# Kernel optimization log

Hardware: AMD Instinct MI355X
Metric: run time of the kernel (lower is better)

## Reference

```python
import jax, jax.numpy as jnp
import numpy as np

B, C, H, W = 32, 256, 64, 64
M, D = 256, 512           # memory_size, memory_dim
NH, HD = 8, 64            # heads, head_dim
EPS = 1e-5


def setup_inputs() -> dict:
    key = jax.random.key(0)
    ks = jax.random.split(key, 12)
    s = 0.02
    return {
        "x": jax.random.normal(ks[0], (B, C, H, W), jnp.float32),
        "memory_bank": jax.random.normal(ks[1], (M, D), jnp.float32),
        "enc_conv_w": jax.random.normal(ks[2], (D // 2, C), jnp.float32) * s,  # 1x1 conv == channel matmul
        "enc_conv_b": jnp.zeros((D // 2,), jnp.float32),
        "bn_gamma": jnp.ones((D // 2,), jnp.float32),
        "bn_beta": jnp.zeros((D // 2,), jnp.float32),
        "bn_mean": jnp.zeros((D // 2,), jnp.float32),
        "bn_var": jnp.ones((D // 2,), jnp.float32),
        "enc_lin_w": jax.random.normal(ks[3], (D, D // 2), jnp.float32) * s,
        "enc_lin_b": jnp.zeros((D,), jnp.float32),
        "ln_gamma": jnp.ones((D,), jnp.float32),
        "ln_beta": jnp.zeros((D,), jnp.float32),
        "attn_in_w": jax.random.normal(ks[4], (3 * D, D), jnp.float32) * s,
        "attn_in_b": jnp.zeros((3 * D,), jnp.float32),
        "attn_out_w": jax.random.normal(ks[5], (D, D), jnp.float32) * s,
        "attn_out_b": jnp.zeros((D,), jnp.float32),
        "gate_w": jax.random.normal(ks[6], (D, 2 * D), jnp.float32) * s,
        "gate_b": jnp.zeros((D,), jnp.float32),
        "rec_w1": jax.random.normal(ks[7], (D // 2, D), jnp.float32) * s,
        "rec_b1": jnp.zeros((D // 2,), jnp.float32),
        "rec_w2": jax.random.normal(ks[8], (C, D // 2), jnp.float32) * s,
        "rec_b2": jnp.zeros((C,), jnp.float32),
        "spat_conv_w": jax.random.normal(ks[9], (1, 2, 7, 7), jnp.float32) * s,
    }


def reference(x, memory_bank, enc_conv_w, enc_conv_b, bn_gamma, bn_beta, bn_mean, bn_var,
              enc_lin_w, enc_lin_b, ln_gamma, ln_beta, attn_in_w, attn_in_b,
              attn_out_w, attn_out_b, gate_w, gate_b, rec_w1, rec_b1, rec_w2, rec_b2,
              spat_conv_w):
    # ---- feature encoder: 1x1 conv -> BN(eval) -> ReLU -> global avg pool -> Linear -> LayerNorm ----
    h = jnp.einsum('bchw,oc->bohw', x, enc_conv_w) + enc_conv_b[None, :, None, None]
    bn_scale = (bn_gamma / jnp.sqrt(bn_var + EPS))[None, :, None, None]
    h = (h - bn_mean[None, :, None, None]) * bn_scale + bn_beta[None, :, None, None]
    h = jax.nn.relu(h)
    h = h.mean(axis=(2, 3))                                   # (B, D//2)
    h = h @ enc_lin_w.T + enc_lin_b                           # (B, D)
    mu = h.mean(-1, keepdims=True)
    var = h.var(-1, keepdims=True)
    enc = (h - mu) / jnp.sqrt(var + EPS) * ln_gamma + ln_beta  # (B, D)

    # ---- memory retrieval: MHA with q_len=1, keys/values = shared memory bank ----
    Wq, Wk, Wv = jnp.split(attn_in_w, 3, axis=0)
    bq, bk, bv = jnp.split(attn_in_b, 3)
    q = (enc @ Wq.T + bq).reshape(B, NH, HD)                  # (B, H, d)
    k = (memory_bank @ Wk.T + bk).reshape(M, NH, HD)          # (M, H, d) — batch-shared
    v = (memory_bank @ Wv.T + bv).reshape(M, NH, HD)
    scores = jnp.einsum('bhd,mhd->bhm', q, k) / np.float32(np.sqrt(HD))
    att = jax.nn.softmax(scores, axis=-1)                     # (B, H, M)
    ctx = jnp.einsum('bhm,mhd->bhd', att, v).reshape(B, D)
    retrieved = ctx @ attn_out_w.T + attn_out_b               # (B, D)

    # ---- gated fusion ----
    gate = jax.nn.sigmoid(jnp.concatenate([enc, retrieved], axis=-1) @ gate_w.T + gate_b)
    fused = gate * enc + (1.0 - gate) * retrieved             # (B, D)

    # ---- per-channel weights from fused features ----
    sw = jax.nn.sigmoid(jax.nn.relu(fused @ rec_w1.T + rec_b1) @ rec_w2.T + rec_b2)  # (B, C)

    # ---- spatial attention on [avg, max] channel stats ----
    avg = x.mean(axis=1, keepdims=True)
    mx = x.max(axis=1, keepdims=True)
    sp_in = jnp.concatenate([avg, mx], axis=1)                # (B, 2, H, W)
    sa = jax.lax.conv_general_dilated(sp_in, spat_conv_w, (1, 1), [(3, 3), (3, 3)],
                                      dimension_numbers=('NCHW', 'OIHW', 'NCHW'))
    sa = jax.nn.sigmoid(sa)                                   # (B, 1, H, W)

    return x * sw[:, :, None, None] * sa                      # (B, C, H, W)
```

## Files before the change

kernel.cpp:

```cpp
#include <hip/hip_runtime.h>
#include <math.h>

#define EPSV 1e-5f

typedef __attribute__((ext_vector_type(8))) short short8;
typedef __attribute__((ext_vector_type(8))) unsigned short ushort8;
typedef __attribute__((ext_vector_type(4))) float f32x4;

__device__ __forceinline__ unsigned short f2bf(float f){
  unsigned u = __builtin_bit_cast(unsigned, f);
  u += 0x7fffu + ((u >> 16) & 1u);
  return (unsigned short)(u >> 16);
}
__device__ __forceinline__ float dot4f(float4 w, const float* v){
  return w.x*v[0] + w.y*v[1] + w.z*v[2] + w.w*v[3];
}
__device__ __forceinline__ float sigmoidf(float v){ return 1.f/(1.f + expf(-v)); }

__global__ __launch_bounds__(256) void k_pack(const float* __restrict__ w1,
                                              const float* __restrict__ wattn,
                                              unsigned short* __restrict__ p1,
                                              unsigned short* __restrict__ pkv){
  const int total1 = 256*256, total2 = 1024*512;
  for (int idx = blockIdx.x*256 + threadIdx.x; idx < total1 + total2; idx += gridDim.x*256){
    if (idx < total1){
      int o = idx >> 8, c = idx & 255;
      int off = (((o>>4)*8 + (c>>5))*64 + (((c>>3)&3)*16 + (o&15)))*8 + (c&7);
      p1[off] = f2bf(w1[idx]);
    } else {
      int j = idx - total1; int o = j >> 9, c = j & 511;
      int off = (((o>>4)*16 + (c>>5))*64 + (((c>>3)&3)*16 + (o&15)))*8 + (c&7);
      pkv[off] = f2bf(wattn[512*512 + j]);
    }
  }
}

__global__ __launch_bounds__(256) void k_conv(
    const float* __restrict__ x, const unsigned short* __restrict__ wp,
    const float* __restrict__ cb, const float* __restrict__ bng,
    const float* __restrict__ bnb, const float* __restrict__ bnm,
    const float* __restrict__ bnv,
    float* __restrict__ ppool, float* __restrict__ wavg, float* __restrict__ wmax){
  int bid = blockIdx.x;
  int b = bid >> 6, tile = bid & 63;
  int px0 = tile << 6;
  int t = threadIdx.x;
  int lane = t & 63, wv = t >> 6;
  int px = t & 63, cg = wv;
  __shared__ __align__(16) unsigned short a_lds[16384];
  __shared__ float st_s[256], st_m[256];

  const float* xb = x + (size_t)b*(256*4096) + px0 + px;

  float ssum = 0.f, smax = -3.4e38f;
  const unsigned wbase = (((px >> 4) << 6) + ((unsigned)cg << 4) + (px & 15)) << 4;

  #pragma unroll
  for (int ch = 0; ch < 8; ++ch){
    float xv[8];
    #pragma unroll
    for (int u = 0; u < 8; ++u)
      xv[u] = __builtin_nontemporal_load(xb + (size_t)(ch*32 + cg*8 + u) * 4096);
    ushort8 pk;
    #pragma unroll
    for (int u = 0; u < 8; ++u){
      ssum += xv[u];
      smax = fmaxf(smax, xv[u]);
      pk[u] = f2bf(xv[u]);
    }
    *(ushort8*)((char*)a_lds + wbase + (ch << 12)) = pk;
  }
  st_s[t] = ssum; st_m[t] = smax;
  __syncthreads();

  if (t < 64){
    float s = st_s[t] + st_s[t+64] + st_s[t+128] + st_s[t+192];
    float m = fmaxf(fmaxf(st_m[t], st_m[t+64]), fmaxf(st_m[t+128], st_m[t+192]));
    wavg[(b << 12) + px0 + t] = s * (1.f/256.f);
    wmax[(b << 12) + px0 + t] = m;
  }

  f32x4 acc[4][4];
  #pragma unroll
  for (int i = 0; i < 4; ++i)
    #pragma unroll
    for (int j = 0; j < 4; ++j){ f32x4 z = {0.f,0.f,0.f,0.f}; acc[i][j] = z; }

  #pragma unroll
  for (int ch = 0; ch < 8; ++ch){
    short8 afr[4];
    #pragma unroll
    for (int mf = 0; mf < 4; ++mf)
      afr[mf] = *(const short8*)((const char*)a_lds + (ch << 12) + (mf << 10) + lane*16);
    #pragma unroll
    for (int nf = 0; nf < 4; ++nf){
      short8 bfr = *(const short8*)(wp + (size_t)(((wv*4 + nf)*8 + ch) * 512 + lane*8));
      #pragma unroll
      for (int mf = 0; mf < 4; ++mf)
        acc[mf][nf] = __builtin_amdgcn_mfma_f32_16x16x32_bf16(afr[mf], bfr, acc[mf][nf], 0, 0, 0);
    }
  }

  #pragma unroll
  for (int nf = 0; nf < 4; ++nf){
    int o = (wv << 6) + (nf << 4) + (lane & 15);
    float sc = bng[o] * rsqrtf(bnv[o] + EPSV);
    float sh = bnb[o] + (cb[o] - bnm[o]) * sc;
    float ps = 0.f;
    #pragma unroll
    for (int mf = 0; mf < 4; ++mf)
      #pragma unroll
      for (int r = 0; r < 4; ++r)
        ps += fmaxf(acc[mf][nf][r] * sc + sh, 0.f);
    ps += __shfl_xor(ps, 16, 64);
    ps += __shfl_xor(ps, 32, 64);
    if ((lane & 48) == 0)
      ppool[(size_t)((b << 6) + tile)*256 + o] = ps;
  }
}

__global__ __launch_bounds__(256) void k_enc(const float* __restrict__ pp,
    const float* __restrict__ lw, const float* __restrict__ lb,
    const float* __restrict__ lng, const float* __restrict__ lnb,
    float* __restrict__ enc){
  int b = blockIdx.x, t = threadIdx.x;
  __shared__ __align__(16) float p_s[256];
  __shared__ float h_s[512], red[8];
  float s = 0.f;
  for (int tile = 0; tile < 64; ++tile) s += pp[(size_t)((b<<6)+tile)*256 + t];
  p_s[t] = s * (1.f/4096.f);
  __syncthreads();
  float hv[2];
  #pragma unroll
  for (int k = 0; k < 2; ++k){
    int d = t + k*256;
    const float4* wr = (const float4*)(lw + (size_t)d*256);
    float a = 0.f;
    for (int j = 0; j < 64; ++j) a += dot4f(wr[j], &p_s[4*j]);
    hv[k] = a + lb[d];
    h_s[d] = hv[k];
  }
  float ls = hv[0] + hv[1], lq = hv[0]*hv[0] + hv[1]*hv[1];
  #pragma unroll
  for (int msk = 1; msk < 64; msk <<= 1){
    ls += __shfl_xor(ls, msk, 64);
    lq += __shfl_xor(lq, msk, 64);
  }
  if ((t & 63) == 0){ red[t>>6] = ls; red[4 + (t>>6)] = lq; }
  __syncthreads();
  float su = red[0]+red[1]+red[2]+red[3];
  float sq = red[4]+red[5]+red[6]+red[7];
  float mu = su * (1.f/512.f);
  float vr = sq * (1.f/512.f) - mu*mu;
  float rstd = rsqrtf(vr + EPSV);
  #pragma unroll
  for (int k = 0; k < 2; ++k){
    int d = t + k*256;
    enc[(size_t)b*512 + d] = (h_s[d] - mu)*rstd*lng[d] + lnb[d];
  }
}

__global__ __launch_bounds__(256) void k_kv(const float* __restrict__ mb,
    const unsigned short* __restrict__ wp, const float* __restrict__ attb,
    float* __restrict__ kvb){
  int bid = blockIdx.x;
  int mt = bid >> 4, nt = bid & 15;
  int m0 = mt << 4;
  int mu = nt >> 3;
  int ncol0 = (nt & 7) << 6;
  int t = threadIdx.x, lane = t & 63, wv = t >> 6;
  int l15 = lane & 15, l4 = lane >> 4;

  const float* arow = mb + (size_t)(m0 + l15)*512 + l4*8;
  int ofrag = (nt << 2) + wv;

  f32x4 acc = {0.f,0.f,0.f,0.f};
  #pragma unroll
  for (int ch = 0; ch < 16; ++ch){
    float4 a0 = *(const float4*)(arow + ch*32);
    float4 a1 = *(const float4*)(arow + ch*32 + 4);
    short8 afr;
    afr[0] = (short)f2bf(a0.x); afr[1] = (short)f2bf(a0.y);
    afr[2] = (short)f2bf(a0.z); afr[3] = (short)f2bf(a0.w);
    afr[4] = (short)f2bf(a1.x); afr[5] = (short)f2bf(a1.y);
    afr[6] = (short)f2bf(a1.z); afr[7] = (short)f2bf(a1.w);
    short8 bfr = *(const short8*)(wp + (size_t)(ofrag*16 + ch)*512 + lane*8);
    acc = __builtin_amdgcn_mfma_f32_16x16x32_bf16(afr, bfr, acc, 0, 0, 0);
  }
  float bias = attb[512 + mu*512 + ncol0 + (wv << 4) + l15];
  #pragma unroll
  for (int i = 0; i < 4; ++i){
    int row = m0 + l4*4 + i;
    int col = ncol0 + (wv << 4) + l15;
    kvb[(size_t)mu*131072 + (size_t)row*512 + col] = acc[i] + bias;
  }
}

__global__ __launch_bounds__(256) void k_qkattn(const float* __restrict__ enc,
    const float* __restrict__ kvb, const float* __restrict__ attw,
    const float* __restrict__ attb, float* __restrict__ ctxout){
  int bid = blockIdx.x;
  int b = bid >> 3, h = bid & 7;
  int t = threadIdx.x;
  __shared__ float e_s[512];
  __shared__ __align__(16) float q_s[64];
  __shared__ float att_s[256];
  __shared__ float red_s[256];
  __shared__ float r2[8];

  e_s[t]       = enc[(size_t)b*512 + t];
  e_s[t + 256] = enc[(size_t)b*512 + 256 + t];
  __syncthreads();

  {
    int i = t >> 2, part = t & 3;
    const float4* wr = (const float4*)(attw + (size_t)(h*64 + i)*512 + part*128);
    const float* ev = e_s + part*128;
    float a = 0.f;
    #pragma unroll
    for (int j = 0; j < 32; ++j) a += dot4f(wr[j], ev + 4*j);
    a += __shfl_xor(a, 1, 64);
    a += __shfl_xor(a, 2, 64);
    if (part == 0) q_s[i] = a + attb[h*64 + i];
  }
  __syncthreads();

  float sc;
  {
    const float4* kr = (const float4*)(kvb + (size_t)t*512 + h*64);
    const float4* qr = (const float4*)q_s;
    float a = 0.f;
    #pragma unroll
    for (int j = 0; j < 16; ++j){
      float4 kk = kr[j], qq = qr[j];
      a += kk.x*qq.x + kk.y*qq.y + kk.z*qq.z + kk.w*qq.w;
    }
    sc = a * 0.125f;
  }
  int wv = t >> 6, lane = t & 63;
  float mx = sc;
  #pragma unroll
  for (int msk = 1; msk < 64; msk <<= 1) mx = fmaxf(mx, __shfl_xor(mx, msk, 64));
  if (lane == 0) r2[wv] = mx;
  __syncthreads();
  mx = fmaxf(fmaxf(r2[0], r2[1]), fmaxf(r2[2], r2[3]));
  float ex = expf(sc - mx);
  float sum = ex;
  #pragma unroll
  for (int msk = 1; msk < 64; msk <<= 1) sum += __shfl_xor(sum, msk, 64);
  if (lane == 0) r2[4 + wv] = sum;
  __syncthreads();
  float inv = 1.f / (r2[4] + r2[5] + r2[6] + r2[7]);
  att_s[t] = ex * inv;
  __syncthreads();

  {
    const float* vbase = kvb + 131072 + (size_t)(wv*64)*512 + h*64 + lane;
    const float* at = att_s + wv*64;
    float a = 0.f;
    #pragma unroll 8
    for (int m = 0; m < 64; ++m) a += at[m] * vbase[(size_t)m*512];
    red_s[wv*64 + lane] = a;
  }
  __syncthreads();
  if (t < 64)
    ctxout[(size_t)b*512 + h*64 + t] = red_s[t] + red_s[64+t] + red_s[128+t] + red_s[192+t];
}

__global__ __launch_bounds__(256) void k_outproj(const float* __restrict__ ctx,
    const float* __restrict__ ow, const float* __restrict__ obv,
    float* __restrict__ retr){
  int bid = blockIdx.x;
  int b = bid >> 3, n0 = (bid & 7) << 6;
  int t = threadIdx.x;
  __shared__ float c_s[512];
  c_s[t]       = ctx[(size_t)b*512 + t];
  c_s[t + 256] = ctx[(size_t)b*512 + 256 + t];
  __syncthreads();
  int o = n0 + (t >> 2), part = t & 3;
  const float4* wr = (const float4*)(ow + (size_t)o*512 + part*128);
  const float* cv = c_s + part*128;
  float a = 0.f;
  #pragma unroll
  for (int j = 0; j < 32; ++j) a += dot4f(wr[j], cv + 4*j);
  a += __shfl_xor(a, 1, 64);
  a += __shfl_xor(a, 2, 64);
  if (part == 0) retr[(size_t)b*512 + o] = a + obv[o];
}

__global__ __launch_bounds__(256) void k_gate(const float* __restrict__ enc,
    const float* __restrict__ retr, const float* __restrict__ gw,
    const float* __restrict__ gb, float* __restrict__ fused){
  int bid = blockIdx.x;
  int b = bid >> 3, n0 = (bid & 7) << 6;
  int t = threadIdx.x;
  __shared__ float ef[1024];
  ef[t]        = enc[(size_t)b*512 + t];
  ef[t + 256]  = enc[(size_t)b*512 + 256 + t];
  ef[t + 512]  = retr[(size_t)b*512 + t];
  ef[t + 768]  = retr[(size_t)b*512 + 256 + t];
  __syncthreads();
  int o = n0 + (t >> 2), part = t & 3;
  const float4* wr = (const float4*)(gw + (size_t)o*1024 + part*256);
  const float* fv = ef + part*256;
  float a = 0.f;
  #pragma unroll
  for (int j = 0; j < 64; ++j) a += dot4f(wr[j], fv + 4*j);
  a += __shfl_xor(a, 1, 64);
  a += __shfl_xor(a, 2, 64);
  if (part == 0){
    float g = sigmoidf(a + gb[o]);
    fused[(size_t)b*512 + o] = g*ef[o] + (1.f - g)*ef[512 + o];
  }
}

__global__ __launch_bounds__(256) void k_rec1(const float* __restrict__ fused,
    const float* __restrict__ r1w, const float* __restrict__ r1b,
    float* __restrict__ t1){
  int bid = blockIdx.x;
  int b = bid >> 2, n0 = (bid & 3) << 6;
  int t = threadIdx.x;
  __shared__ float f_s[512];
  f_s[t]       = fused[(size_t)b*512 + t];
  f_s[t + 256] = fused[(size_t)b*512 + 256 + t];
  __syncthreads();
  int o = n0 + (t >> 2), part = t & 3;
  const float4* wr = (const float4*)(r1w + (size_t)o*512 + part*128);
  const float* fv = f_s + part*128;
  float a = 0.f;
  #pragma unroll
  for (int j = 0; j < 32; ++j) a += dot4f(wr[j], fv + 4*j);
  a += __shfl_xor(a, 1, 64);
  a += __shfl_xor(a, 2, 64);
  if (part == 0) t1[(size_t)b*256 + o] = fmaxf(a + r1b[o], 0.f);
}

__global__ __launch_bounds__(256) void k_rec2(const float* __restrict__ t1,
    const float* __restrict__ r2w, const float* __restrict__ r2b,
    float* __restrict__ swout){
  int bid = blockIdx.x;
  int b = bid >> 2, n0 = (bid & 3) << 6;
  int t = threadIdx.x;
  __shared__ float t_s[256];
  t_s[t] = t1[(size_t)b*256 + t];
  __syncthreads();
  int o = n0 + (t >> 2), part = t & 3;
  const float4* wr = (const float4*)(r2w + (size_t)o*256 + part*64);
  const float* tv = t_s + part*64;
  float a = 0.f;
  #pragma unroll
  for (int j = 0; j < 16; ++j) a += dot4f(wr[j], tv + 4*j);
  a += __shfl_xor(a, 1, 64);
  a += __shfl_xor(a, 2, 64);
  if (part == 0) swout[(size_t)b*256 + o] = sigmoidf(a + r2b[o]);
}

__global__ __launch_bounds__(256) void k_spconv(const float* __restrict__ wavg,
    const float* __restrict__ wmax, const float* __restrict__ wgt,
    float* __restrict__ sa){
  __shared__ float w_s[98];
  int t = threadIdx.x;
  if (t < 98) w_s[t] = wgt[t];
  __syncthreads();
  int b = blockIdx.x >> 4;
  int px = ((blockIdx.x & 15) << 8) + t;
  int y = px >> 6, xx = px & 63;
  const float* pa = wavg + (b << 12);
  const float* pm = wmax + (b << 12);
  float a = 0.f;
  #pragma unroll
  for (int ky = 0; ky < 7; ++ky){
    int yy = y + ky - 3;
    if (yy < 0 || yy >= 64) continue;
    #pragma unroll
    for (int kx = 0; kx < 7; ++kx){
      int x2 = xx + kx - 3;
      if (x2 < 0 || x2 >= 64) continue;
      int o = (yy << 6) + x2;
      a += pa[o]*w_s[ky*7+kx] + pm[o]*w_s[49+ky*7+kx];
    }
  }
  sa[(b << 12) + px] = sigmoidf(a);
}

__global__ __launch_bounds__(256) void k_final(const float* __restrict__ x,
    const float* __restrict__ sw, const float* __restrict__ sa,
    float* __restrict__ out){
  const size_t total = 8388608;
  for (size_t q = (size_t)blockIdx.x*256 + threadIdx.x; q < total; q += (size_t)gridDim.x*256){
    size_t b = q >> 18;
    int c = (int)((q >> 10) & 255);
    int p4 = (int)(q & 1023);
    f32x4 xv = __builtin_nontemporal_load((const f32x4*)x + q);
    f32x4 sv = ((const f32x4*)sa)[(b << 10) + p4];
    float s = sw[(b << 8) + c];
    f32x4 o = xv * s * sv;
    __builtin_nontemporal_store(o, (f32x4*)out + q);
  }
}

extern "C" void kernel_launch(void* const* d_in, const int* in_sizes, int n_in,
                              void* d_out, int out_size, void* d_ws, size_t ws_size,
                              hipStream_t stream){
  const float* x    = (const float*)d_in[0];
  const float* mb   = (const float*)d_in[1];
  const float* w1   = (const float*)d_in[2];
  const float* cbv  = (const float*)d_in[3];
  const float* bng  = (const float*)d_in[4];
  const float* bnb  = (const float*)d_in[5];
  const float* bnm  = (const float*)d_in[6];
  const float* bnv  = (const float*)d_in[7];
  const float* lw   = (const float*)d_in[8];
  const float* lb   = (const float*)d_in[9];
  const float* lng  = (const float*)d_in[10];
  const float* lnb  = (const float*)d_in[11];
  const float* attw = (const float*)d_in[12];
  const float* attb = (const float*)d_in[13];
  const float* ow   = (const float*)d_in[14];
  const float* obv  = (const float*)d_in[15];
  const float* gw   = (const float*)d_in[16];
  const float* gb   = (const float*)d_in[17];
  const float* r1w  = (const float*)d_in[18];
  const float* r1b  = (const float*)d_in[19];
  const float* r2w  = (const float*)d_in[20];
  const float* r2b  = (const float*)d_in[21];
  const float* spw  = (const float*)d_in[22];
  float* out = (float*)d_out;

  char* ws = (char*)d_ws;
  unsigned short* w1p  = (unsigned short*)(ws + 0);
  unsigned short* wkvp = (unsigned short*)(ws + 131072);
  float* ppool = (float*)(ws + 1179648);
  float* wavg  = (float*)(ws + 3276800);
  float* wmax  = (float*)(ws + 3801088);
  float* encb  = (float*)(ws + 4325376);
  float* kvb   = (float*)(ws + 4390912);
  float* swb   = (float*)(ws + 5439488);
  float* sab   = (float*)(ws + 5472256);
  float* ctxb  = (float*)(ws + 5996544);
  float* retrb = (float*)(ws + 6062080);
  float* fusedb= (float*)(ws + 6127616);
  float* t1b   = (float*)(ws + 6193152);

  k_pack   <<<2304, 256, 0, stream>>>(w1, attw, w1p, wkvp);
  k_conv   <<<2048, 256, 0, stream>>>(x, w1p, cbv, bng, bnb, bnm, bnv, ppool, wavg, wmax);
  k_enc    <<<32,   256, 0, stream>>>(ppool, lw, lb, lng, lnb, encb);
  k_kv     <<<256,  256, 0, stream>>>(mb, wkvp, attb, kvb);
  k_qkattn <<<256,  256, 0, stream>>>(encb, kvb, attw, attb, ctxb);
  k_outproj<<<256,  256, 0, stream>>>(ctxb, ow, obv, retrb);
  k_gate   <<<256,  256, 0, stream>>>(encb, retrb, gw, gb, fusedb);
  k_rec1   <<<128,  256, 0, stream>>>(fusedb, r1w, r1b, t1b);
  k_rec2   <<<128,  256, 0, stream>>>(t1b, r2w, r2b, swb);
  k_spconv <<<512,  256, 0, stream>>>(wavg, wmax, spw, sab);
  k_final  <<<2048, 256, 0, stream>>>(x, swb, sab, out);
}
```

Baseline: 176.6 us.

## Fuse encoder LayerNorm into attention and merge tail MLPs into one kernel

Removes the standalone encoder kernel by recomputing the pooled-feature linear plus LayerNorm inside each attention block. It also fuses out-projection, gating, and both reconstruction layers into a single per-batch 512-thread kernel. Four launches and the global round-trips of intermediates go away. In exchange the encoder matvec is computed redundantly eight times per batch, and the tail runs on only 32 blocks, each thread streaming full weight rows, so parallelism across the device is much lower.

```diff
diff --git a/kernel.cpp b/kernel.cpp
--- a/kernel.cpp
+++ b/kernel.cpp
@@ -119,47 +119,6 @@
   }
 }
 
-__global__ __launch_bounds__(256) void k_enc(const float* __restrict__ pp,
-    const float* __restrict__ lw, const float* __restrict__ lb,
-    const float* __restrict__ lng, const float* __restrict__ lnb,
-    float* __restrict__ enc){
-  int b = blockIdx.x, t = threadIdx.x;
-  __shared__ __align__(16) float p_s[256];
-  __shared__ float h_s[512], red[8];
-  float s = 0.f;
-  for (int tile = 0; tile < 64; ++tile) s += pp[(size_t)((b<<6)+tile)*256 + t];
-  p_s[t] = s * (1.f/4096.f);
-  __syncthreads();
-  float hv[2];
-  #pragma unroll
-  for (int k = 0; k < 2; ++k){
-    int d = t + k*256;
-    const float4* wr = (const float4*)(lw + (size_t)d*256);
-    float a = 0.f;
-    for (int j = 0; j < 64; ++j) a += dot4f(wr[j], &p_s[4*j]);
-    hv[k] = a + lb[d];
-    h_s[d] = hv[k];
-  }
-  float ls = hv[0] + hv[1], lq = hv[0]*hv[0] + hv[1]*hv[1];
-  #pragma unroll
-  for (int msk = 1; msk < 64; msk <<= 1){
-    ls += __shfl_xor(ls, msk, 64);
-    lq += __shfl_xor(lq, msk, 64);
-  }
-  if ((t & 63) == 0){ red[t>>6] = ls; red[4 + (t>>6)] = lq; }
-  __syncthreads();
-  float su = red[0]+red[1]+red[2]+red[3];
-  float sq = red[4]+red[5]+red[6]+red[7];
-  float mu = su * (1.f/512.f);
-  float vr = sq * (1.f/512.f) - mu*mu;
-  float rstd = rsqrtf(vr + EPSV);
-  #pragma unroll
-  for (int k = 0; k < 2; ++k){
-    int d = t + k*256;
-    enc[(size_t)b*512 + d] = (h_s[d] - mu)*rstd*lng[d] + lnb[d];
-  }
-}
-
 __global__ __launch_bounds__(256) void k_kv(const float* __restrict__ mb,
     const unsigned short* __restrict__ wp, const float* __restrict__ attb,
     float* __restrict__ kvb){
@@ -196,20 +155,56 @@
   }
 }
 
-__global__ __launch_bounds__(256) void k_qkattn(const float* __restrict__ enc,
+__global__ __launch_bounds__(256) void k_qkattn(const float* __restrict__ pp,
+    const float* __restrict__ lw, const float* __restrict__ lb,
+    const float* __restrict__ lng, const float* __restrict__ lnb,
     const float* __restrict__ kvb, const float* __restrict__ attw,
     const float* __restrict__ attb, float* __restrict__ ctxout){
   int bid = blockIdx.x;
   int b = bid >> 3, h = bid & 7;
   int t = threadIdx.x;
+  __shared__ __align__(16) float p_s[256];
   __shared__ float e_s[512];
   __shared__ __align__(16) float q_s[64];
   __shared__ float att_s[256];
   __shared__ float red_s[256];
   __shared__ float r2[8];
 
-  e_s[t]       = enc[(size_t)b*512 + t];
-  e_s[t + 256] = enc[(size_t)b*512 + 256 + t];
+  {
+    float s = 0.f;
+    for (int tile = 0; tile < 64; ++tile) s += pp[(size_t)((b<<6)+tile)*256 + t];
+    p_s[t] = s * (1.f/4096.f);
+  }
+  __syncthreads();
+  {
+    float hv[2];
+    #pragma unroll
+    for (int k = 0; k < 2; ++k){
+      int d = t + k*256;
+      const float4* wr = (const float4*)(lw + (size_t)d*256);
+      float a = 0.f;
+      for (int j = 0; j < 64; ++j) a += dot4f(wr[j], &p_s[4*j]);
+      hv[k] = a + lb[d];
+    }
+    float ls = hv[0] + hv[1], lq = hv[0]*hv[0] + hv[1]*hv[1];
+    #pragma unroll
+    for (int msk = 1; msk < 64; msk <<= 1){
+      ls += __shfl_xor(ls, msk, 64);
+      lq += __shfl_xor(lq, msk, 64);
+    }
+    if ((t & 63) == 0){ r2[t>>6] = ls; r2[4 + (t>>6)] = lq; }
+    __syncthreads();
+    float su = r2[0]+r2[1]+r2[2]+r2[3];
+    float sq = r2[4]+r2[5]+r2[6]+r2[7];
+    float mu = su * (1.f/512.f);
+    float vr = sq * (1.f/512.f) - mu*mu;
+    float rstd = rsqrtf(vr + EPSV);
+    #pragma unroll
+    for (int k = 0; k < 2; ++k){
+      int d = t + k*256;
+      e_s[d] = (hv[k] - mu)*rstd*lng[d] + lnb[d];
+    }
+  }
   __syncthreads();
 
   {
@@ -241,6 +236,7 @@
   float mx = sc;
   #pragma unroll
   for (int msk = 1; msk < 64; msk <<= 1) mx = fmaxf(mx, __shfl_xor(mx, msk, 64));
+  __syncthreads();
   if (lane == 0) r2[wv] = mx;
   __syncthreads();
   mx = fmaxf(fmaxf(r2[0], r2[1]), fmaxf(r2[2], r2[3]));
@@ -267,92 +263,92 @@
     ctxout[(size_t)b*512 + h*64 + t] = red_s[t] + red_s[64+t] + red_s[128+t] + red_s[192+t];
 }
 
-__global__ __launch_bounds__(256) void k_outproj(const float* __restrict__ ctx,
+__global__ __launch_bounds__(512) void k_tail(
+    const float* __restrict__ pp,
+    const float* __restrict__ lw, const float* __restrict__ lb,
+    const float* __restrict__ lng, const float* __restrict__ lnb,
+    const float* __restrict__ ctx,
     const float* __restrict__ ow, const float* __restrict__ obv,
-    float* __restrict__ retr){
-  int bid = blockIdx.x;
-  int b = bid >> 3, n0 = (bid & 7) << 6;
-  int t = threadIdx.x;
-  __shared__ float c_s[512];
-  c_s[t]       = ctx[(size_t)b*512 + t];
-  c_s[t + 256] = ctx[(size_t)b*512 + 256 + t];
-  __syncthreads();
-  int o = n0 + (t >> 2), part = t & 3;
-  const float4* wr = (const float4*)(ow + (size_t)o*512 + part*128);
-  const float* cv = c_s + part*128;
-  float a = 0.f;
-  #pragma unroll
-  for (int j = 0; j < 32; ++j) a += dot4f(wr[j], cv + 4*j);
-  a += __shfl_xor(a, 1, 64);
-  a += __shfl_xor(a, 2, 64);
-  if (part == 0) retr[(size_t)b*512 + o] = a + obv[o];
-}
-
-__global__ __launch_bounds__(256) void k_gate(const float* __restrict__ enc,
-    const float* __restrict__ retr, const float* __restrict__ gw,
-    const float* __restrict__ gb, float* __restrict__ fused){
-  int bid = blockIdx.x;
-  int b = bid >> 3, n0 = (bid & 7) << 6;
-  int t = threadIdx.x;
-  __shared__ float ef[1024];
-  ef[t]        = enc[(size_t)b*512 + t];
-  ef[t + 256]  = enc[(size_t)b*512 + 256 + t];
-  ef[t + 512]  = retr[(size_t)b*512 + t];
-  ef[t + 768]  = retr[(size_t)b*512 + 256 + t];
-  __syncthreads();
-  int o = n0 + (t >> 2), part = t & 3;
-  const float4* wr = (const float4*)(gw + (size_t)o*1024 + part*256);
-  const float* fv = ef + part*256;
-  float a = 0.f;
-  #pragma unroll
-  for (int j = 0; j < 64; ++j) a += dot4f(wr[j], fv + 4*j);
-  a += __shfl_xor(a, 1, 64);
-  a += __shfl_xor(a, 2, 64);
-  if (part == 0){
-    float g = sigmoidf(a + gb[o]);
-    fused[(size_t)b*512 + o] = g*ef[o] + (1.f - g)*ef[512 + o];
-  }
-}
-
-__global__ __launch_bounds__(256) void k_rec1(const float* __restrict__ fused,
+    const float* __restrict__ gw, const float* __restrict__ gb,
     const float* __restrict__ r1w, const float* __restrict__ r1b,
-    float* __restrict__ t1){
-  int bid = blockIdx.x;
-  int b = bid >> 2, n0 = (bid & 3) << 6;
-  int t = threadIdx.x;
-  __shared__ float f_s[512];
-  f_s[t]       = fused[(size_t)b*512 + t];
-  f_s[t + 256] = fused[(size_t)b*512 + 256 + t];
-  __syncthreads();
-  int o = n0 + (t >> 2), part = t & 3;
-  const float4* wr = (const float4*)(r1w + (size_t)o*512 + part*128);
-  const float* fv = f_s + part*128;
-  float a = 0.f;
-  #pragma unroll
-  for (int j = 0; j < 32; ++j) a += dot4f(wr[j], fv + 4*j);
-  a += __shfl_xor(a, 1, 64);
-  a += __shfl_xor(a, 2, 64);
-  if (part == 0) t1[(size_t)b*256 + o] = fmaxf(a + r1b[o], 0.f);
-}
-
-__global__ __launch_bounds__(256) void k_rec2(const float* __restrict__ t1,
     const float* __restrict__ r2w, const float* __restrict__ r2b,
     float* __restrict__ swout){
-  int bid = blockIdx.x;
-  int b = bid >> 2, n0 = (bid & 3) << 6;
-  int t = threadIdx.x;
-  __shared__ float t_s[256];
-  t_s[t] = t1[(size_t)b*256 + t];
-  __syncthreads();
-  int o = n0 + (t >> 2), part = t & 3;
-  const float4* wr = (const float4*)(r2w + (size_t)o*256 + part*64);
-  const float* tv = t_s + part*64;
-  float a = 0.f;
-  #pragma unroll
-  for (int j = 0; j < 16; ++j) a += dot4f(wr[j], tv + 4*j);
-  a += __shfl_xor(a, 1, 64);
-  a += __shfl_xor(a, 2, 64);
-  if (part == 0) swout[(size_t)b*256 + o] = sigmoidf(a + r2b[o]);
+  int b = blockIdx.x, t = threadIdx.x;
+  int wv = t >> 6;
+  __shared__ __align__(16) float p_s[256];
+  __shared__ __align__(16) float c_s[512];
+  __shared__ __align__(16) float e_s[512];
+  __shared__ __align__(16) float r_s[512];
+  __shared__ __align__(16) float f_s[512];
+  __shared__ __align__(16) float t_s[256];
+  __shared__ float red[16];
+
+  c_s[t] = ctx[(size_t)b*512 + t];
+  if (t < 256){
+    float s = 0.f;
+    for (int tile = 0; tile < 64; ++tile) s += pp[(size_t)((b<<6)+tile)*256 + t];
+    p_s[t] = s * (1.f/4096.f);
+  }
+  __syncthreads();
+
+  float hv;
+  {
+    const float4* wr = (const float4*)(lw + (size_t)t*256);
+    float a = 0.f;
+    for (int j = 0; j < 64; ++j) a += dot4f(wr[j], &p_s[4*j]);
+    hv = a + lb[t];
+  }
+  {
+    float ls = hv, lq = hv*hv;
+    #pragma unroll
+    for (int msk = 1; msk < 64; msk <<= 1){
+      ls += __shfl_xor(ls, msk, 64);
+      lq += __shfl_xor(lq, msk, 64);
+    }
+    if ((t & 63) == 0){ red[wv] = ls; red[8 + wv] = lq; }
+    __syncthreads();
+    float su = 0.f, sq = 0.f;
+    #pragma unroll
+    for (int w = 0; w < 8; ++w){ su += red[w]; sq += red[8 + w]; }
+    float mu = su * (1.f/512.f);
+    float vr = sq * (1.f/512.f) - mu*mu;
+    float rstd = rsqrtf(vr + EPSV);
+    e_s[t] = (hv - mu)*rstd*lng[t] + lnb[t];
+  }
+  __syncthreads();
+
+  {
+    const float4* wr = (const float4*)(ow + (size_t)t*512);
+    float a = 0.f;
+    for (int j = 0; j < 128; ++j) a += dot4f(wr[j], &c_s[4*j]);
+    r_s[t] = a + obv[t];
+  }
+  __syncthreads();
+
+  {
+    const float4* wr = (const float4*)(gw + (size_t)t*1024);
+    float a = 0.f;
+    for (int j = 0; j < 128; ++j) a += dot4f(wr[j], &e_s[4*j]);
+    for (int j = 0; j < 128; ++j) a += dot4f(wr[128 + j], &r_s[4*j]);
+    float g = sigmoidf(a + gb[t]);
+    f_s[t] = g*e_s[t] + (1.f - g)*r_s[t];
+  }
+  __syncthreads();
+
+  if (t < 256){
+    const float4* wr = (const float4*)(r1w + (size_t)t*512);
+    float a = 0.f;
+    for (int j = 0; j < 128; ++j) a += dot4f(wr[j], &f_s[4*j]);
+    t_s[t] = fmaxf(a + r1b[t], 0.f);
+  }
+  __syncthreads();
+
+  if (t < 256){
+    const float4* wr = (const float4*)(r2w + (size_t)t*256);
+    float a = 0.f;
+    for (int j = 0; j < 64; ++j) a += dot4f(wr[j], &t_s[4*j]);
+    swout[(size_t)b*256 + t] = sigmoidf(a + r2b[t]);
+  }
 }
 
 __global__ __launch_bounds__(256) void k_spconv(const float* __restrict__ wavg,
@@ -433,24 +429,17 @@
   float* ppool = (float*)(ws + 1179648);
   float* wavg  = (float*)(ws + 3276800);
   float* wmax  = (float*)(ws + 3801088);
-  float* encb  = (float*)(ws + 4325376);
   float* kvb   = (float*)(ws + 4390912);
   float* swb   = (float*)(ws + 5439488);
   float* sab   = (float*)(ws + 5472256);
   float* ctxb  = (float*)(ws + 5996544);
-  float* retrb = (float*)(ws + 6062080);
-  float* fusedb= (float*)(ws + 6127616);
-  float* t1b   = (float*)(ws + 6193152);
 
   k_pack   <<<2304, 256, 0, stream>>>(w1, attw, w1p, wkvp);
   k_conv   <<<2048, 256, 0, stream>>>(x, w1p, cbv, bng, bnb, bnm, bnv, ppool, wavg, wmax);
-  k_enc    <<<32,   256, 0, stream>>>(ppool, lw, lb, lng, lnb, encb);
   k_kv     <<<256,  256, 0, stream>>>(mb, wkvp, attb, kvb);
-  k_qkattn <<<256,  256, 0, stream>>>(encb, kvb, attw, attb, ctxb);
-  k_outproj<<<256,  256, 0, stream>>>(ctxb, ow, obv, retrb);
-  k_gate   <<<256,  256, 0, stream>>>(encb, retrb, gw, gb, fusedb);
-  k_rec1   <<<128,  256, 0, stream>>>(fusedb, r1w, r1b, t1b);
-  k_rec2   <<<128,  256, 0, stream>>>(t1b, r2w, r2b, swb);
+  k_qkattn <<<256,  256, 0, stream>>>(ppool, lw, lb, lng, lnb, kvb, attw, attb, ctxb);
+  k_tail   <<<32,   512, 0, stream>>>(ppool, lw, lb, lng, lnb, ctxb, ow, obv,
+                                      gw, gb, r1w, r1b, r2w, r2b, swb);
   k_spconv <<<512,  256, 0, stream>>>(wavg, wmax, spw, sab);
   k_final  <<<2048, 256, 0, stream>>>(x, swb, sab, out);
 }
```

Result: slower. 271.7 us (+53.8%).
